# Kernel optimization log

Hardware: AMD Instinct MI355X
Metric: run time of the kernel (lower is better)

## Reference

```python
import jax, jax.numpy as jnp
import numpy as np

B, S = 512, 64          # batch, grain grid size (coarse==medium==fine==64, see notes)
N = S * S               # tokens per image
CONTENT_PAD, CONTENT_EOS = 1024, 1025
COARSE_POS_PAD, COARSE_POS_EOS = 128, 129
MEDIUM_POS_PAD, MEDIUM_POS_EOS = 256, 257
FINE_POS_PAD, FINE_POS_EOS = 1024, 1025


def setup_inputs() -> dict:
    key = jax.random.key(0)
    k1, k2 = jax.random.split(key)
    indices = jax.random.randint(k1, (B, S, S), 0, 1024, dtype=jnp.int32)
    grain_indices = jax.random.randint(k2, (B, S, S), 0, 3, dtype=jnp.int32)
    return {"indices": indices, "grain_indices": grain_indices}


def _compact(vals, mask, eos, pad):
    """Stable stream-compaction per row: selected vals first, then EOS, then PAD.
    vals/mask: [B, N].  Output: [B, N+1] (static max length; torch pads to batch max)."""
    b, n = vals.shape
    # stable argsort of (not mask) brings True positions to the front, in order
    order = jnp.argsort(jnp.where(mask, 0, 1).astype(jnp.int32), axis=1, stable=True)
    sel = jnp.take_along_axis(vals, order, axis=1)                  # [B, N]
    sel = jnp.concatenate([sel, jnp.zeros((b, 1), vals.dtype)], axis=1)  # [B, N+1]
    cnt = jnp.sum(mask.astype(jnp.int32), axis=1, keepdims=True)    # [B, 1]
    slot = jnp.arange(n + 1, dtype=jnp.int32)[None, :]              # [1, N+1]
    out = jnp.where(slot < cnt, sel,
                    jnp.where(slot == cnt, jnp.asarray(eos, vals.dtype),
                              jnp.asarray(pad, vals.dtype)))
    return out


def reference(indices, grain_indices):
    b, s, _ = indices.shape
    n = s * s
    # With coarse==medium==fine the module's rearranges are identity reshapes:
    # coarse_content = medium_content source = fine_content source = flattened grid,
    # and all three position sequences are row-major arange(n).
    flat = indices.reshape(b, n)
    g = grain_indices.reshape(b, n)
    pos = jnp.broadcast_to(jnp.arange(n, dtype=indices.dtype), (b, n))

    coarse_content = _compact(flat, g == 0, CONTENT_EOS, CONTENT_PAD)
    coarse_position = _compact(pos, g == 0, COARSE_POS_EOS, COARSE_POS_PAD)
    medium_content = _compact(flat, g == 1, CONTENT_EOS, CONTENT_PAD)
    medium_position = _compact(pos, g == 1, MEDIUM_POS_EOS, MEDIUM_POS_PAD)
    fine_content = _compact(flat, g == 2, CONTENT_EOS, CONTENT_PAD)
    fine_position = _compact(pos, g == 2, FINE_POS_EOS, FINE_POS_PAD)

    coarse_segment = jnp.zeros_like(coarse_content)
    medium_segment = jnp.ones_like(medium_content)
    fine_segment = jnp.full_like(fine_content, 2)
    return (coarse_content, medium_content, fine_content,
            coarse_position, medium_position, fine_position,
            coarse_segment, medium_segment, fine_segment)
```

## Files before the change

### kernel.cpp

```cpp
#include <hip/hip_runtime.h>


constexpr int N_TOK  = 4096;
constexpr int M_OUT  = N_TOK + 1;
constexpr int TPB    = 1024;
constexpr int NWAVES = TPB / 64;
constexpr int EPT    = N_TOK / TPB;

constexpr int CONTENT_PAD = 1024, CONTENT_EOS = 1025;
__device__ __constant__ int POS_PAD[3] = {128, 256, 1024};
__device__ __constant__ int POS_EOS[3] = {129, 257, 1025};

__global__ __launch_bounds__(TPB, 8) void
triple_grain_permute(const int* __restrict__ indices,
                     const int* __restrict__ grain,
                     int* __restrict__ out,
                     int batch) {
    const int b = blockIdx.x;
    const int t = threadIdx.x;
    const int lane = t & 63;
    const int wave = t >> 6;

    const int* idx_row = indices + (size_t)b * N_TOK;
    const int* g_row   = grain   + (size_t)b * N_TOK;

    __shared__ int s_packed[N_TOK];
    __shared__ unsigned int s_wave_tot[NWAVES];

    int4 gg = reinterpret_cast<const int4*>(g_row)[t];
    int4 ii = reinterpret_cast<const int4*>(idx_row)[t];
    int gv[EPT] = {gg.x, gg.y, gg.z, gg.w};
    const int elem0 = t * EPT;
    int pv[EPT] = {ii.x | (elem0 << 12),
                   ii.y | ((elem0 + 1) << 12),
                   ii.z | ((elem0 + 2) << 12),
                   ii.w | ((elem0 + 3) << 12)};

    int c0 = 0, c1 = 0, c2 = 0;
#pragma unroll
    for (int j = 0; j < EPT; ++j) {
        c0 += (gv[j] == 0);
        c1 += (gv[j] == 1);
        c2 += (gv[j] == 2);
    }
    unsigned int packed = (unsigned)c0 | ((unsigned)c1 << 10) | ((unsigned)c2 << 20);

    unsigned int inc = packed;
#pragma unroll
    for (int off = 1; off < 64; off <<= 1) {
        unsigned int nb = (unsigned int)__shfl_up((int)inc, off, 64);
        if (lane >= off) inc += nb;
    }
    if (lane == 63) s_wave_tot[wave] = inc;
    __syncthreads();

    int wp0 = 0, wp1 = 0, wp2 = 0, tot0 = 0, tot1 = 0, tot2 = 0;
#pragma unroll
    for (int w = 0; w < NWAVES; ++w) {
        const unsigned int v = s_wave_tot[w];
        const int f0 = v & 1023, f1 = (v >> 10) & 1023, f2 = (v >> 20) & 1023;
        if (w < wave) { wp0 += f0; wp1 += f1; wp2 += f2; }
        tot0 += f0; tot1 += f1; tot2 += f2;
    }
    const unsigned int exv = inc - packed;
    const int o0 = wp0 + (int)(exv & 1023);
    const int o1 = wp1 + (int)((exv >> 10) & 1023);
    const int o2 = wp2 + (int)((exv >> 20) & 1023);
    const int cnt0 = tot0, cnt1 = tot1, cnt2 = tot2;

    const int base0 = 0, base1 = cnt0, base2 = cnt0 + cnt1;

    int d0 = base0 + o0, d1 = base1 + o1, d2 = base2 + o2;
#pragma unroll
    for (int j = 0; j < EPT; ++j) {
        const int c = gv[j];
        const int dst = (c == 0) ? d0 : ((c == 1) ? d1 : d2);
        s_packed[dst] = pv[j];
        d0 += (c == 0);
        d1 += (c == 1);
        d2 += (c == 2);
    }
    __syncthreads();

    const size_t ARR = (size_t)batch * M_OUT;
    const int peel = (4 - (b & 3)) & 3;
    const int nch  = (M_OUT - peel) >> 2;
    const int rem  = (M_OUT - peel) & 3;

    const int bases[3] = {base0, base1, base2};
    const int cnts[3]  = {cnt0, cnt1, cnt2};

#pragma unroll
    for (int c = 0; c < 3; ++c) {
        int* dst_c = out + (size_t)c       * ARR + (size_t)b * M_OUT;
        int* dst_p = out + (size_t)(3 + c) * ARR + (size_t)b * M_OUT;
        int* dst_s = out + (size_t)(6 + c) * ARR + (size_t)b * M_OUT;
        const int cnt = cnts[c];
        const int base = bases[c];
        const int peos = POS_EOS[c], ppad = POS_PAD[c];

        auto elem = [&](int slot, int& vc, int& vp) {
            int a = base + slot;
            a = (a > N_TOK - 1) ? (N_TOK - 1) : a;
            const int pk = s_packed[a];
            vc = (slot < cnt) ? (pk & 0xFFF) : ((slot == cnt) ? CONTENT_EOS : CONTENT_PAD);
            vp = (slot < cnt) ? (pk >> 12)   : ((slot == cnt) ? peos : ppad);
        };

        if (t < peel) {
            int vc, vp;
            elem(t, vc, vp);
            dst_c[t] = vc; dst_p[t] = vp; dst_s[t] = c;
        }
        if (t < nch) {
            const int s0 = peel + 4 * t;
            int4 vc4, vp4;
            elem(s0 + 0, vc4.x, vp4.x);
            elem(s0 + 1, vc4.y, vp4.y);
            elem(s0 + 2, vc4.z, vp4.z);
            elem(s0 + 3, vc4.w, vp4.w);
            *reinterpret_cast<int4*>(dst_c + s0) = vc4;
            *reinterpret_cast<int4*>(dst_p + s0) = vp4;
            *reinterpret_cast<int4*>(dst_s + s0) = make_int4(c, c, c, c);
        }
        if (t < rem) {
            const int slot = M_OUT - rem + t;
            int vc, vp;
            elem(slot, vc, vp);
            dst_c[slot] = vc; dst_p[slot] = vp; dst_s[slot] = c;
        }
    }
}

extern "C" void kernel_launch(void* const* d_in, const int* in_sizes, int n_in,
                              void* d_out, int out_size, void* d_ws, size_t ws_size,
                              hipStream_t stream) {
    const int* indices = (const int*)d_in[0];
    const int* grain   = (const int*)d_in[1];
    int* out = (int*)d_out;

    const int batch = in_sizes[0] / N_TOK;
    triple_grain_permute<<<batch, TPB, 0, stream>>>(indices, grain, out, batch);
}
```

Measured before the change: 91.10 us.

## Issue constant segment and pad stores early, swizzle LDS, lighten barriers

Segment-id outputs are written right after the input loads, and pure-PAD chunks of the content and position outputs are written before the scatter. This overlaps much of the global store traffic with the scan and scatter phases. The LDS index is XOR-swizzled to reduce bank conflicts, and full-valid chunks use a branch-free path. __syncthreads is replaced with an explicit lgkmcnt wait plus s_barrier, which avoids waiting on outstanding global stores at each barrier.

```diff
diff --git a/kernel.cpp b/kernel.cpp
--- a/kernel.cpp
+++ b/kernel.cpp
@@ -10,6 +10,8 @@
 constexpr int CONTENT_PAD = 1024, CONTENT_EOS = 1025;
 __device__ __constant__ int POS_PAD[3] = {128, 256, 1024};
 __device__ __constant__ int POS_EOS[3] = {129, 257, 1025};
+
+__device__ __forceinline__ int swz(int a) { return a ^ ((a >> 3) & 0x1C); }
 
 __global__ __launch_bounds__(TPB, 8) void
 triple_grain_permute(const int* __restrict__ indices,
@@ -27,8 +29,23 @@
     __shared__ int s_packed[N_TOK];
     __shared__ unsigned int s_wave_tot[NWAVES];
 
-    int4 gg = reinterpret_cast<const int4*>(g_row)[t];
-    int4 ii = reinterpret_cast<const int4*>(idx_row)[t];
+    const int4 gg = reinterpret_cast<const int4*>(g_row)[t];
+    const int4 ii = reinterpret_cast<const int4*>(idx_row)[t];
+
+    const size_t ARR = (size_t)batch * M_OUT;
+    const int peel = (4 - (b & 3)) & 3;
+    const int nch  = (M_OUT - peel) >> 2;
+    const int rem  = (M_OUT - peel) & 3;
+    const int s0   = peel + 4 * t;
+
+#pragma unroll
+    for (int c = 0; c < 3; ++c) {
+        int* dst_s = out + (size_t)(6 + c) * ARR + (size_t)b * M_OUT;
+        if (t < peel) dst_s[t] = c;
+        if (t < nch)  *reinterpret_cast<int4*>(dst_s + s0) = make_int4(c, c, c, c);
+        if (t < rem)  dst_s[M_OUT - rem + t] = c;
+    }
+
     int gv[EPT] = {gg.x, gg.y, gg.z, gg.w};
     const int elem0 = t * EPT;
     int pv[EPT] = {ii.x | (elem0 << 12),
@@ -52,7 +69,10 @@
         if (lane >= off) inc += nb;
     }
     if (lane == 63) s_wave_tot[wave] = inc;
-    __syncthreads();
+
+    asm volatile("s_waitcnt lgkmcnt(0)" ::: "memory");
+    __builtin_amdgcn_s_barrier();
+    __builtin_amdgcn_sched_barrier(0);
 
     int wp0 = 0, wp1 = 0, wp2 = 0, tot0 = 0, tot1 = 0, tot2 = 0;
 #pragma unroll
@@ -67,34 +87,42 @@
     const int o1 = wp1 + (int)((exv >> 10) & 1023);
     const int o2 = wp2 + (int)((exv >> 20) & 1023);
     const int cnt0 = tot0, cnt1 = tot1, cnt2 = tot2;
-
     const int base0 = 0, base1 = cnt0, base2 = cnt0 + cnt1;
-
-    int d0 = base0 + o0, d1 = base1 + o1, d2 = base2 + o2;
-#pragma unroll
-    for (int j = 0; j < EPT; ++j) {
-        const int c = gv[j];
-        const int dst = (c == 0) ? d0 : ((c == 1) ? d1 : d2);
-        s_packed[dst] = pv[j];
-        d0 += (c == 0);
-        d1 += (c == 1);
-        d2 += (c == 2);
-    }
-    __syncthreads();
-
-    const size_t ARR = (size_t)batch * M_OUT;
-    const int peel = (4 - (b & 3)) & 3;
-    const int nch  = (M_OUT - peel) >> 2;
-    const int rem  = (M_OUT - peel) & 3;
 
     const int bases[3] = {base0, base1, base2};
     const int cnts[3]  = {cnt0, cnt1, cnt2};
 
 #pragma unroll
     for (int c = 0; c < 3; ++c) {
+        if (t < nch && s0 > cnts[c]) {
+            int* dst_c = out + (size_t)c       * ARR + (size_t)b * M_OUT;
+            int* dst_p = out + (size_t)(3 + c) * ARR + (size_t)b * M_OUT;
+            *reinterpret_cast<int4*>(dst_c + s0) =
+                make_int4(CONTENT_PAD, CONTENT_PAD, CONTENT_PAD, CONTENT_PAD);
+            const int pp = POS_PAD[c];
+            *reinterpret_cast<int4*>(dst_p + s0) = make_int4(pp, pp, pp, pp);
+        }
+    }
+
+    int d0 = base0 + o0, d1 = base1 + o1, d2 = base2 + o2;
+#pragma unroll
+    for (int j = 0; j < EPT; ++j) {
+        const int cl = gv[j];
+        const int dst = (cl == 0) ? d0 : ((cl == 1) ? d1 : d2);
+        s_packed[swz(dst)] = pv[j];
+        d0 += (cl == 0);
+        d1 += (cl == 1);
+        d2 += (cl == 2);
+    }
+
+    asm volatile("s_waitcnt lgkmcnt(0)" ::: "memory");
+    __builtin_amdgcn_s_barrier();
+    __builtin_amdgcn_sched_barrier(0);
+
+#pragma unroll
+    for (int c = 0; c < 3; ++c) {
         int* dst_c = out + (size_t)c       * ARR + (size_t)b * M_OUT;
         int* dst_p = out + (size_t)(3 + c) * ARR + (size_t)b * M_OUT;
-        int* dst_s = out + (size_t)(6 + c) * ARR + (size_t)b * M_OUT;
         const int cnt = cnts[c];
         const int base = bases[c];
         const int peos = POS_EOS[c], ppad = POS_PAD[c];
@@ -102,7 +130,7 @@
         auto elem = [&](int slot, int& vc, int& vp) {
             int a = base + slot;
             a = (a > N_TOK - 1) ? (N_TOK - 1) : a;
-            const int pk = s_packed[a];
+            const int pk = s_packed[swz(a)];
             vc = (slot < cnt) ? (pk & 0xFFF) : ((slot == cnt) ? CONTENT_EOS : CONTENT_PAD);
             vp = (slot < cnt) ? (pk >> 12)   : ((slot == cnt) ? peos : ppad);
         };
@@ -110,24 +138,34 @@
         if (t < peel) {
             int vc, vp;
             elem(t, vc, vp);
-            dst_c[t] = vc; dst_p[t] = vp; dst_s[t] = c;
+            dst_c[t] = vc; dst_p[t] = vp;
         }
         if (t < nch) {
-            const int s0 = peel + 4 * t;
-            int4 vc4, vp4;
-            elem(s0 + 0, vc4.x, vp4.x);
-            elem(s0 + 1, vc4.y, vp4.y);
-            elem(s0 + 2, vc4.z, vp4.z);
-            elem(s0 + 3, vc4.w, vp4.w);
-            *reinterpret_cast<int4*>(dst_c + s0) = vc4;
-            *reinterpret_cast<int4*>(dst_p + s0) = vp4;
-            *reinterpret_cast<int4*>(dst_s + s0) = make_int4(c, c, c, c);
+            if (s0 + 3 < cnt) {
+                const int a = base + s0;
+                const int p0 = s_packed[swz(a)];
+                const int p1 = s_packed[swz(a + 1)];
+                const int p2 = s_packed[swz(a + 2)];
+                const int p3 = s_packed[swz(a + 3)];
+                *reinterpret_cast<int4*>(dst_c + s0) =
+                    make_int4(p0 & 0xFFF, p1 & 0xFFF, p2 & 0xFFF, p3 & 0xFFF);
+                *reinterpret_cast<int4*>(dst_p + s0) =
+                    make_int4(p0 >> 12, p1 >> 12, p2 >> 12, p3 >> 12);
+            } else if (s0 <= cnt) {
+                int4 vc4, vp4;
+                elem(s0 + 0, vc4.x, vp4.x);
+                elem(s0 + 1, vc4.y, vp4.y);
+                elem(s0 + 2, vc4.z, vp4.z);
+                elem(s0 + 3, vc4.w, vp4.w);
+                *reinterpret_cast<int4*>(dst_c + s0) = vc4;
+                *reinterpret_cast<int4*>(dst_p + s0) = vp4;
+            }
         }
         if (t < rem) {
             const int slot = M_OUT - rem + t;
             int vc, vp;
             elem(slot, vc, vp);
-            dst_c[slot] = vc; dst_p[slot] = vp; dst_s[slot] = c;
+            dst_c[slot] = vc; dst_p[slot] = vp;
         }
     }
 }
```

New measurement: 108.4 us. +19.0%, slower.

## Scatter compacted tokens directly to global memory, dropping the LDS staging pass

Applied to the files above, without the earlier changes.

Each token is now written straight from registers to its compacted rank in the global content and position outputs, so the shared-memory buffer and the second barrier are gone. Only the EOS/PAD tail is filled afterwards, and the constant segment arrays are written at kernel start. This removes the LDS round trip and a sync, but the main writes become scattered 4-byte global stores instead of coalesced int4 stores, which may raise memory-transaction cost. The launch-bounds occupancy hint is also lowered from 8 to 4.

```diff
diff --git a/kernel.cpp b/kernel.cpp
--- a/kernel.cpp
+++ b/kernel.cpp
@@ -11,7 +11,7 @@
 __device__ __constant__ int POS_PAD[3] = {128, 256, 1024};
 __device__ __constant__ int POS_EOS[3] = {129, 257, 1025};
 
-__global__ __launch_bounds__(TPB, 8) void
+__global__ __launch_bounds__(TPB, 4) void
 triple_grain_permute(const int* __restrict__ indices,
                      const int* __restrict__ grain,
                      int* __restrict__ out,
@@ -24,17 +24,28 @@
     const int* idx_row = indices + (size_t)b * N_TOK;
     const int* g_row   = grain   + (size_t)b * N_TOK;
 
-    __shared__ int s_packed[N_TOK];
     __shared__ unsigned int s_wave_tot[NWAVES];
 
-    int4 gg = reinterpret_cast<const int4*>(g_row)[t];
-    int4 ii = reinterpret_cast<const int4*>(idx_row)[t];
-    int gv[EPT] = {gg.x, gg.y, gg.z, gg.w};
+    const int4 gg = reinterpret_cast<const int4*>(g_row)[t];
+    const int4 ii = reinterpret_cast<const int4*>(idx_row)[t];
+
+    const size_t ARR = (size_t)batch * M_OUT;
+    const int peel = (4 - (b & 3)) & 3;
+    const int nch  = (M_OUT - peel) >> 2;
+    const int rem  = (M_OUT - peel) & 3;
+    const int s0   = peel + 4 * t;
+
+#pragma unroll
+    for (int c = 0; c < 3; ++c) {
+        int* dst_s = out + (size_t)(6 + c) * ARR + (size_t)b * M_OUT;
+        if (t < peel) dst_s[t] = c;
+        if (t < nch)  *reinterpret_cast<int4*>(dst_s + s0) = make_int4(c, c, c, c);
+        if (t < rem)  dst_s[M_OUT - rem + t] = c;
+    }
+
+    const int gv[EPT] = {gg.x, gg.y, gg.z, gg.w};
+    const int iv[EPT] = {ii.x, ii.y, ii.z, ii.w};
     const int elem0 = t * EPT;
-    int pv[EPT] = {ii.x | (elem0 << 12),
-                   ii.y | ((elem0 + 1) << 12),
-                   ii.z | ((elem0 + 2) << 12),
-                   ii.w | ((elem0 + 3) << 12)};
 
     int c0 = 0, c1 = 0, c2 = 0;
 #pragma unroll
@@ -43,7 +54,8 @@
         c1 += (gv[j] == 1);
         c2 += (gv[j] == 2);
     }
-    unsigned int packed = (unsigned)c0 | ((unsigned)c1 << 10) | ((unsigned)c2 << 20);
+    const unsigned int packed =
+        (unsigned)c0 | ((unsigned)c1 << 10) | ((unsigned)c2 << 20);
 
     unsigned int inc = packed;
 #pragma unroll
@@ -63,72 +75,51 @@
         tot0 += f0; tot1 += f1; tot2 += f2;
     }
     const unsigned int exv = inc - packed;
-    const int o0 = wp0 + (int)(exv & 1023);
-    const int o1 = wp1 + (int)((exv >> 10) & 1023);
-    const int o2 = wp2 + (int)((exv >> 20) & 1023);
-    const int cnt0 = tot0, cnt1 = tot1, cnt2 = tot2;
+    int r0 = wp0 + (int)(exv & 1023);
+    int r1 = wp1 + (int)((exv >> 10) & 1023);
+    int r2 = wp2 + (int)((exv >> 20) & 1023);
+    const int cnts[3] = {tot0, tot1, tot2};
 
-    const int base0 = 0, base1 = cnt0, base2 = cnt0 + cnt1;
-
-    int d0 = base0 + o0, d1 = base1 + o1, d2 = base2 + o2;
 #pragma unroll
     for (int j = 0; j < EPT; ++j) {
         const int c = gv[j];
-        const int dst = (c == 0) ? d0 : ((c == 1) ? d1 : d2);
-        s_packed[dst] = pv[j];
-        d0 += (c == 0);
-        d1 += (c == 1);
-        d2 += (c == 2);
+        const int rank = (c == 0) ? r0 : ((c == 1) ? r1 : r2);
+        int* dc = out + (size_t)c       * ARR + (size_t)b * M_OUT;
+        int* dp = out + (size_t)(3 + c) * ARR + (size_t)b * M_OUT;
+        dc[rank] = iv[j];
+        dp[rank] = elem0 + j;
+        r0 += (c == 0);
+        r1 += (c == 1);
+        r2 += (c == 2);
     }
-    __syncthreads();
-
-    const size_t ARR = (size_t)batch * M_OUT;
-    const int peel = (4 - (b & 3)) & 3;
-    const int nch  = (M_OUT - peel) >> 2;
-    const int rem  = (M_OUT - peel) & 3;
-
-    const int bases[3] = {base0, base1, base2};
-    const int cnts[3]  = {cnt0, cnt1, cnt2};
 
 #pragma unroll
     for (int c = 0; c < 3; ++c) {
-        int* dst_c = out + (size_t)c       * ARR + (size_t)b * M_OUT;
-        int* dst_p = out + (size_t)(3 + c) * ARR + (size_t)b * M_OUT;
-        int* dst_s = out + (size_t)(6 + c) * ARR + (size_t)b * M_OUT;
+        int* dc = out + (size_t)c       * ARR + (size_t)b * M_OUT;
+        int* dp = out + (size_t)(3 + c) * ARR + (size_t)b * M_OUT;
         const int cnt = cnts[c];
-        const int base = bases[c];
         const int peos = POS_EOS[c], ppad = POS_PAD[c];
 
-        auto elem = [&](int slot, int& vc, int& vp) {
-            int a = base + slot;
-            a = (a > N_TOK - 1) ? (N_TOK - 1) : a;
-            const int pk = s_packed[a];
-            vc = (slot < cnt) ? (pk & 0xFFF) : ((slot == cnt) ? CONTENT_EOS : CONTENT_PAD);
-            vp = (slot < cnt) ? (pk >> 12)   : ((slot == cnt) ? peos : ppad);
+        auto fillone = [&](int slot) {
+            if (slot == cnt)      { dc[slot] = CONTENT_EOS; dp[slot] = peos; }
+            else if (slot > cnt)  { dc[slot] = CONTENT_PAD; dp[slot] = ppad; }
         };
 
-        if (t < peel) {
-            int vc, vp;
-            elem(t, vc, vp);
-            dst_c[t] = vc; dst_p[t] = vp; dst_s[t] = c;
+        if (t < peel) fillone(t);
+        if (t < nch) {
+            if (s0 > cnt) {
+                *reinterpret_cast<int4*>(dc + s0) =
+                    make_int4(CONTENT_PAD, CONTENT_PAD, CONTENT_PAD, CONTENT_PAD);
+                *reinterpret_cast<int4*>(dp + s0) =
+                    make_int4(ppad, ppad, ppad, ppad);
+            } else if (s0 + 3 >= cnt) {
+                fillone(s0 + 0);
+                fillone(s0 + 1);
+                fillone(s0 + 2);
+                fillone(s0 + 3);
+            }
         }
-        if (t < nch) {
-            const int s0 = peel + 4 * t;
-            int4 vc4, vp4;
-            elem(s0 + 0, vc4.x, vp4.x);
-            elem(s0 + 1, vc4.y, vp4.y);
-            elem(s0 + 2, vc4.z, vp4.z);
-            elem(s0 + 3, vc4.w, vp4.w);
-            *reinterpret_cast<int4*>(dst_c + s0) = vc4;
-            *reinterpret_cast<int4*>(dst_p + s0) = vp4;
-            *reinterpret_cast<int4*>(dst_s + s0) = make_int4(c, c, c, c);
-        }
-        if (t < rem) {
-            const int slot = M_OUT - rem + t;
-            int vc, vp;
-            elem(slot, vc, vp);
-            dst_c[slot] = vc; dst_p[slot] = vp; dst_s[slot] = c;
-        }
+        if (t < rem) fillone(M_OUT - rem + t);
     }
 }
 
```

Result: slower. 96.53 us (+6.0%).
